# Kernel tuning notes

Hardware: AMD Instinct MI355X
Metric: run time of the kernel (lower is better)

The kernel has to match this reference:

```python
import jax, jax.numpy as jnp
import numpy as np

N = 100000   # nodes
E = 1600000  # edges
F_IN = 256   # input features
H = 128      # hidden
C = 40       # classes


def setup_inputs() -> dict:
    key = jax.random.key(0)
    ks = jax.random.split(key, 6)
    x = jax.random.normal(ks[0], (N, F_IN), dtype=jnp.float32)
    edge_index = jax.random.randint(ks[1], (2, E), 0, N, dtype=jnp.int32)
    edge_attr = jax.random.uniform(ks[2], (E,), dtype=jnp.float32)
    # Glorot-style init like GCNConv
    W1 = jax.random.normal(ks[3], (F_IN, H), dtype=jnp.float32) * (1.0 / np.sqrt(F_IN))
    b1 = jnp.zeros((H,), dtype=jnp.float32)
    W2 = jax.random.normal(ks[4], (H, C), dtype=jnp.float32) * (1.0 / np.sqrt(H))
    b2 = jnp.zeros((C,), dtype=jnp.float32)
    return {"x": x, "edge_index": edge_index, "edge_attr": edge_attr,
            "W1": W1, "b1": b1, "W2": W2, "b2": b2}


def _gcn_norm(edge_index, edge_weight, num_nodes):
    # PyG gcn_norm: add self-loops (weight 1), symmetric D^{-1/2} A D^{-1/2}
    row, col = edge_index[0], edge_index[1]
    loop = jnp.arange(num_nodes, dtype=row.dtype)
    row = jnp.concatenate([row, loop])
    col = jnp.concatenate([col, loop])
    ew = jnp.concatenate([edge_weight, jnp.ones((num_nodes,), edge_weight.dtype)])
    deg = jax.ops.segment_sum(ew, col, num_segments=num_nodes)
    dinv = jnp.where(deg > 0, jax.lax.rsqrt(deg), 0.0)
    norm = dinv[row] * ew * dinv[col]
    return row, col, norm


def _gcn_conv(x, row, col, norm, W, b):
    h = x @ W                              # [N, out] dense transform first
    msg = h[row] * norm[:, None]           # gather source + edge scaling
    out = jax.ops.segment_sum(msg, col, num_segments=x.shape[0])  # scatter-add
    return out + b


def reference(x, edge_index, edge_attr, W1, b1, W2, b2):
    row, col, norm = _gcn_norm(edge_index, edge_attr, x.shape[0])
    h = _gcn_conv(x, row, col, norm, W1, b1)
    h = jax.nn.relu(h)
    # dropout is identity in eval mode
    h = _gcn_conv(h, row, col, norm, W2, b2)
    return jax.nn.log_softmax(h, axis=1)
```

## Files before the change

### kernel.cpp

```cpp
#include <hip/hip_runtime.h>

#define N_NODES 100000
#define N_EDGES 1600000
#define F_INPUT 256
#define H_DIM   128
#define C_DIM   40
#define NB1     ((N_NODES + 255) / 256)
#define NGEMM1  1563
#define NCOUNT  1563
#define NMEGA   (NGEMM1 + NCOUNT)
#define PSTR    32

typedef short  bf8   __attribute__((ext_vector_type(8)));
typedef float  f32x4 __attribute__((ext_vector_type(4)));
typedef float  f32x2 __attribute__((ext_vector_type(2)));
typedef unsigned short u16x8 __attribute__((ext_vector_type(8)));

static __device__ __forceinline__ unsigned short f2bf(float f) {
    union { float f; unsigned u; } v; v.f = f;
    unsigned r = v.u + 0x7FFFu + ((v.u >> 16) & 1u);
    return (unsigned short)(r >> 16);
}
static __device__ __forceinline__ float bf2f(unsigned short b) {
    union { unsigned u; float f; } v; v.u = ((unsigned)b) << 16;
    return v.f;
}
static __device__ __forceinline__ f32x2 bfpair(unsigned u) {
    union { unsigned u; float f; } lo, hi;
    lo.u = u << 16; hi.u = u & 0xFFFF0000u;
    return (f32x2){lo.f, hi.f};
}

__global__ void k_pre(unsigned* packed, const float* __restrict__ W1,
                      const float* __restrict__ W2,
                      unsigned short* Wp1, unsigned short* Wp2) {
    if (blockIdx.x < NB1) {
        int i = blockIdx.x * 256 + threadIdx.x;
        if (i < N_NODES) packed[(size_t)i * PSTR] = (1u << 16);
        return;
    }
    int idx = (blockIdx.x - NB1) * 256 + threadIdx.x;
    if (idx < 32768) {
        int j = idx & 7, lane = (idx >> 3) & 63, ks = (idx >> 9) & 7, nt = idx >> 12;
        int m = lane & 15, q = lane >> 4;
        Wp1[idx] = f2bf(W1[(ks * 32 + q * 8 + j) * H_DIM + nt * 16 + m]);
    }
    int idx2 = idx - 32768;
    if (idx2 >= 0 && idx2 < 6144) {
        int j = idx2 & 7, lane = (idx2 >> 3) & 63, ks = (idx2 >> 9) & 3, nt = idx2 >> 11;
        int m = lane & 15, q = lane >> 4;
        int n = nt * 16 + m;
        Wp2[idx2] = (n < C_DIM) ? f2bf(W2[(ks * 32 + q * 8 + j) * C_DIM + n]) : (unsigned short)0;
    }
}

__global__ __launch_bounds__(256, 4) void k_mega(
        const float* __restrict__ x, const unsigned short* __restrict__ Wp,
        unsigned short* __restrict__ h,
        const int* __restrict__ col, const float* __restrict__ ea,
        unsigned* packed, int* __restrict__ rank) {
    __shared__ unsigned short lds_out[64 * H_DIM];
    int b = blockIdx.x;
    bool is_gemm = ((b & 1) == 0);
    if (!is_gemm) {
        int cb = b >> 1;
        int e0 = cb * 1024 + threadIdx.x;
        int cs[4]; unsigned qs[4]; unsigned old[4];
#pragma unroll
        for (int k = 0; k < 4; k++) {
            int e = e0 + k * 256;
            if (e < N_EDGES) {
                cs[k] = col[e];
                qs[k] = __float2uint_rn(ea[e] * 65536.0f);
            } else cs[k] = -1;
        }
#pragma unroll
        for (int k = 0; k < 4; k++)
            if (cs[k] >= 0)
                old[k] = atomicAdd(packed + (size_t)cs[k] * PSTR, (1u << 24) | qs[k]);
#pragma unroll
        for (int k = 0; k < 4; k++) {
            int e = e0 + k * 256;
            if (e < N_EDGES) rank[e] = (int)(old[k] >> 24);
        }
        return;
    }
    int tile = b >> 1;
    int tid = threadIdx.x;
    int wave = tid >> 6, lane = tid & 63;
    int m = lane & 15, q = lane >> 4;
    int row0 = tile * 64 + wave * 16;
    int rowA = row0 + m; if (rowA >= N_NODES) rowA = N_NODES - 1;

    f32x4 acc[8];
#pragma unroll
    for (int i = 0; i < 8; i++) acc[i] = (f32x4){0.f, 0.f, 0.f, 0.f};
    const float* xr = x + (long)rowA * F_INPUT + q * 8;
#pragma unroll
    for (int ks = 0; ks < 8; ks++) {
        float4 a0 = *(const float4*)(xr + ks * 32);
        float4 a1 = *(const float4*)(xr + ks * 32 + 4);
        bf8 a;
        a[0] = (short)f2bf(a0.x); a[1] = (short)f2bf(a0.y);
        a[2] = (short)f2bf(a0.z); a[3] = (short)f2bf(a0.w);
        a[4] = (short)f2bf(a1.x); a[5] = (short)f2bf(a1.y);
        a[6] = (short)f2bf(a1.z); a[7] = (short)f2bf(a1.w);
#pragma unroll
        for (int nt = 0; nt < 8; nt++) {
            bf8 bb = *(const bf8*)(Wp + (((nt * 8 + ks) * 64 + lane) << 3));
            acc[nt] = __builtin_amdgcn_mfma_f32_16x16x32_bf16(a, bb, acc[nt], 0, 0, 0);
        }
    }
    int lrow = wave * 16 + q * 4;
#pragma unroll
    for (int nt = 0; nt < 8; nt++)
#pragma unroll
        for (int r = 0; r < 4; r++)
            lds_out[(lrow + r) * H_DIM + nt * 16 + m] = f2bf(acc[nt][r]);
    __syncthreads();
    int valid = N_NODES - tile * 64; if (valid > 64) valid = 64;
    unsigned short* gbase = h + (size_t)tile * 64 * H_DIM;
#pragma unroll
    for (int i = 0; i < 4; i++) {
        int idx = (i * 256 + tid) * 8;
        if (idx < valid * H_DIM)
            *(u16x8*)(gbase + idx) = *(const u16x8*)(lds_out + idx);
    }
}

__global__ void k_scan1(const unsigned* __restrict__ packed, int* start, int* bsum,
                        float* dinv, int* __restrict__ cnt) {
    __shared__ int s[256];
    int i = blockIdx.x * 256 + threadIdx.x;
    unsigned pk = (i < N_NODES) ? packed[(size_t)i * PSTR] : 0;
    if (i < N_NODES) {
        dinv[i] = rsqrtf((float)(pk & 0xFFFFFFu) * (1.0f / 65536.0f));
        cnt[i] = (int)(pk >> 24);
    }
    int v = (int)(pk >> 24);
    s[threadIdx.x] = v; __syncthreads();
    for (int off = 1; off < 256; off <<= 1) {
        int t = (threadIdx.x >= off) ? s[threadIdx.x - off] : 0;
        __syncthreads();
        s[threadIdx.x] += t;
        __syncthreads();
    }
    if (i < N_NODES) start[i] = s[threadIdx.x] - v;
    if (threadIdx.x == 255) bsum[blockIdx.x] = s[255];
}

__global__ void k_scan2(int* bsum) {
    __shared__ int s[512];
    int v = (threadIdx.x < NB1) ? bsum[threadIdx.x] : 0;
    s[threadIdx.x] = v; __syncthreads();
    for (int off = 1; off < 512; off <<= 1) {
        int t = (threadIdx.x >= off) ? s[threadIdx.x - off] : 0;
        __syncthreads();
        s[threadIdx.x] += t;
        __syncthreads();
    }
    if (threadIdx.x < NB1) bsum[threadIdx.x] = s[threadIdx.x] - v;
}

__global__ void k_scatter(const int* __restrict__ row, const int* __restrict__ col,
                          const float* __restrict__ ea, const float* __restrict__ dinv,
                          const int* __restrict__ start, const int* __restrict__ bsum,
                          const int* __restrict__ rank, int2* __restrict__ csr) {
    int e = blockIdx.x * 256 + threadIdx.x;
    if (e < N_EDGES) {
        int c = col[e];
        int r = row[e];
        int pos = start[c] + bsum[c >> 8] + rank[e];
        float w = ea[e] * dinv[r];
        csr[pos] = make_int2(r, __float_as_int(w));
    }
}

__global__ void k_agg1(const unsigned short* __restrict__ h, const int2* __restrict__ csr,
                       const int* __restrict__ start, const int* __restrict__ bsum,
                       const int* __restrict__ cnt,
                       const float* __restrict__ dinv, const float* __restrict__ b1,
                       unsigned short* __restrict__ h1) {
    int c = (blockIdx.x * blockDim.x + threadIdx.x) >> 6;
    int lane = threadIdx.x & 63;
    if (c >= N_NODES) return;
    int eg = lane >> 4, cl = lane & 15;
    float di = dinv[c];
    int s = start[c] + bsum[c >> 8];
    int n = cnt[c];

    float w[5]; int r[5];
#pragma unroll
    for (int t = 0; t < 5; t++) {
        int i = eg + 4 * t;
        int2 p = csr[s + ((i < n) ? i : 0)];
        bool val = (i < n);
        r[t] = val ? p.x : c;
        w[t] = val ? __int_as_float(p.y) : 0.f;
    }
    uint4 gv[5];
#pragma unroll
    for (int t = 0; t < 5; t++)
        gv[t] = *(const uint4*)(h + (long)r[t] * H_DIM + cl * 8);
    uint4 selfv = (eg == 0) ? *(const uint4*)(h + (long)c * H_DIM + cl * 8)
                            : (uint4){0, 0, 0, 0};

    f32x2 acc[4];
#pragma unroll
    for (int k = 0; k < 4; k++) acc[k] = (f32x2){0.f, 0.f};
    {
        unsigned sv[4] = {selfv.x, selfv.y, selfv.z, selfv.w};
        f32x2 dd = (f32x2){di, di};
        if (eg == 0)
#pragma unroll
            for (int k = 0; k < 4; k++) acc[k] += dd * bfpair(sv[k]);
    }
#pragma unroll
    for (int t = 0; t < 5; t++) {
        unsigned vv[4] = {gv[t].x, gv[t].y, gv[t].z, gv[t].w};
        f32x2 ww = (f32x2){w[t], w[t]};
#pragma unroll
        for (int k = 0; k < 4; k++) acc[k] += ww * bfpair(vv[k]);
    }
    for (int i = 20 + eg; i < n; i += 4) {
        int2 p = csr[s + i];
        uint4 v4 = *(const uint4*)(h + (long)p.x * H_DIM + cl * 8);
        unsigned vv[4] = {v4.x, v4.y, v4.z, v4.w};
        float wt = __int_as_float(p.y);
        f32x2 ww = (f32x2){wt, wt};
#pragma unroll
        for (int k = 0; k < 4; k++) acc[k] += ww * bfpair(vv[k]);
    }
#pragma unroll
    for (int k = 0; k < 4; k++) {
        acc[k].x += __shfl_xor(acc[k].x, 16); acc[k].y += __shfl_xor(acc[k].y, 16);
        acc[k].x += __shfl_xor(acc[k].x, 32); acc[k].y += __shfl_xor(acc[k].y, 32);
    }
    if (eg == 0) {
        u16x8 o;
#pragma unroll
        for (int k = 0; k < 4; k++) {
            o[2 * k]     = f2bf(fmaxf(di * acc[k].x + b1[cl * 8 + 2 * k], 0.f));
            o[2 * k + 1] = f2bf(fmaxf(di * acc[k].y + b1[cl * 8 + 2 * k + 1], 0.f));
        }
        *(u16x8*)(h1 + (long)c * H_DIM + cl * 8) = o;
    }
}

__global__ __launch_bounds__(256, 4) void k_gemm2(const unsigned short* __restrict__ h1,
                        const unsigned short* __restrict__ Wp,
                        unsigned short* __restrict__ h2) {
    __shared__ unsigned short lds_out[64 * C_DIM];
    int tid = threadIdx.x;
    int wave = tid >> 6, lane = tid & 63;
    int m = lane & 15, q = lane >> 4;
    int row0 = blockIdx.x * 64 + wave * 16;
    int rowA = row0 + m; if (rowA >= N_NODES) rowA = N_NODES - 1;

    f32x4 acc[3];
#pragma unroll
    for (int i = 0; i < 3; i++) acc[i] = (f32x4){0.f, 0.f, 0.f, 0.f};
    const unsigned short* hr = h1 + (long)rowA * H_DIM + q * 8;
#pragma unroll
    for (int ks = 0; ks < 4; ks++) {
        bf8 a = *(const bf8*)(hr + ks * 32);
#pragma unroll
        for (int nt = 0; nt < 3; nt++) {
            bf8 b = *(const bf8*)(Wp + (((nt * 4 + ks) * 64 + lane) << 3));
            acc[nt] = __builtin_amdgcn_mfma_f32_16x16x32_bf16(a, b, acc[nt], 0, 0, 0);
        }
    }
    int lrow = wave * 16 + q * 4;
#pragma unroll
    for (int nt = 0; nt < 3; nt++)
#pragma unroll
        for (int r = 0; r < 4; r++) {
            int colo = nt * 16 + m;
            if (colo < C_DIM)
                lds_out[(lrow + r) * C_DIM + colo] = f2bf(acc[nt][r]);
        }
    __syncthreads();
    int valid = N_NODES - blockIdx.x * 64; if (valid > 64) valid = 64;
    unsigned short* gbase = h2 + (size_t)blockIdx.x * 64 * C_DIM;
    int total = valid * C_DIM;
#pragma unroll
    for (int i = 0; i < 3; i++) {
        int idx = (i * 256 + tid) * 4;
        if (idx < total)
            *(uint2*)(gbase + idx) = *(const uint2*)(lds_out + idx);
    }
}

__global__ void k_agg2(const unsigned short* __restrict__ h2, const int2* __restrict__ csr,
                       const int* __restrict__ start, const int* __restrict__ bsum,
                       const int* __restrict__ cnt,
                       const float* __restrict__ dinv, const float* __restrict__ b2,
                       float* __restrict__ out) {
    int c = (blockIdx.x * blockDim.x + threadIdx.x) >> 6;
    int lane = threadIdx.x & 63;
    if (c >= N_NODES) return;
    int eg = lane >> 3, cl = lane & 7;
    float di = dinv[c];
    int s = start[c] + bsum[c >> 8];
    int n = cnt[c];

    float w[3]; int r[3];
#pragma unroll
    for (int t = 0; t < 3; t++) {
        int i = eg + 8 * t;
        int2 p = csr[s + ((i < n) ? i : 0)];
        bool val = (i < n);
        r[t] = val ? p.x : c;
        w[t] = val ? __int_as_float(p.y) : 0.f;
    }
    uint4 gv[3] = {{0,0,0,0},{0,0,0,0},{0,0,0,0}};
    uint4 selfv = {0, 0, 0, 0};
    if (cl < 5) {
#pragma unroll
        for (int t = 0; t < 3; t++)
            gv[t] = *(const uint4*)(h2 + (long)r[t] * C_DIM + cl * 8);
        if (eg == 0) selfv = *(const uint4*)(h2 + (long)c * C_DIM + cl * 8);
    }
    f32x2 acc[4];
#pragma unroll
    for (int k = 0; k < 4; k++) acc[k] = (f32x2){0.f, 0.f};
    {
        unsigned sv[4] = {selfv.x, selfv.y, selfv.z, selfv.w};
        f32x2 dd = (f32x2){di, di};
        if (eg == 0 && cl < 5)
#pragma unroll
            for (int k = 0; k < 4; k++) acc[k] += dd * bfpair(sv[k]);
    }
#pragma unroll
    for (int t = 0; t < 3; t++) {
        unsigned vv[4] = {gv[t].x, gv[t].y, gv[t].z, gv[t].w};
        f32x2 ww = (f32x2){w[t], w[t]};
#pragma unroll
        for (int k = 0; k < 4; k++) acc[k] += ww * bfpair(vv[k]);
    }
    for (int i = 24 + eg; i < n; i += 8) {
        int2 p = csr[s + i];
        if (cl < 5) {
            uint4 v4 = *(const uint4*)(h2 + (long)p.x * C_DIM + cl * 8);
            unsigned vv[4] = {v4.x, v4.y, v4.z, v4.w};
            float wt = __int_as_float(p.y);
            f32x2 ww = (f32x2){wt, wt};
#pragma unroll
            for (int k = 0; k < 4; k++) acc[k] += ww * bfpair(vv[k]);
        }
    }
#pragma unroll
    for (int k = 0; k < 4; k++) {
        acc[k].x += __shfl_xor(acc[k].x, 8);  acc[k].y += __shfl_xor(acc[k].y, 8);
        acc[k].x += __shfl_xor(acc[k].x, 16); acc[k].y += __shfl_xor(acc[k].y, 16);
        acc[k].x += __shfl_xor(acc[k].x, 32); acc[k].y += __shfl_xor(acc[k].y, 32);
    }
    float v[8];
    float lm = -INFINITY;
    if (cl < 5) {
#pragma unroll
        for (int k = 0; k < 4; k++) {
            v[2 * k]     = di * acc[k].x + b2[cl * 8 + 2 * k];
            v[2 * k + 1] = di * acc[k].y + b2[cl * 8 + 2 * k + 1];
            lm = fmaxf(lm, fmaxf(v[2 * k], v[2 * k + 1]));
        }
    }
    lm = fmaxf(lm, __shfl_xor(lm, 1));
    lm = fmaxf(lm, __shfl_xor(lm, 2));
    lm = fmaxf(lm, __shfl_xor(lm, 4));
    float ls = 0.f;
    if (cl < 5) {
#pragma unroll
        for (int j = 0; j < 8; j++) ls += __expf(v[j] - lm);
    }
    ls += __shfl_xor(ls, 1);
    ls += __shfl_xor(ls, 2);
    ls += __shfl_xor(ls, 4);
    if (eg == 0 && cl < 5) {
        float lsm = lm + logf(ls);
        f32x4 o0, o1;
#pragma unroll
        for (int j = 0; j < 4; j++) { o0[j] = v[j] - lsm; o1[j] = v[j + 4] - lsm; }
        *(f32x4*)(out + (long)c * C_DIM + cl * 8)     = o0;
        *(f32x4*)(out + (long)c * C_DIM + cl * 8 + 4) = o1;
    }
}

extern "C" void kernel_launch(void* const* d_in, const int* in_sizes, int n_in,
                              void* d_out, int out_size, void* d_ws, size_t ws_size,
                              hipStream_t stream) {
    const float* x  = (const float*)d_in[0];
    const int*   ei = (const int*)d_in[1];
    const float* ea = (const float*)d_in[2];
    const float* W1 = (const float*)d_in[3];
    const float* b1 = (const float*)d_in[4];
    const float* W2 = (const float*)d_in[5];
    const float* b2 = (const float*)d_in[6];
    const int* row = ei;
    const int* col = ei + N_EDGES;

    char* ws = (char*)d_ws;
    size_t off = 0;
    auto alloc = [&](size_t bytes) -> void* {
        void* p = ws + off;
        off = (off + bytes + 255) & ~(size_t)255;
        return p;
    };
    unsigned*       packed = (unsigned*)alloc((size_t)N_NODES * PSTR * 4);
    float*          dinv   = (float*)alloc((size_t)N_NODES * 4);
    int*            rank   = (int*)alloc((size_t)N_EDGES * 4);
    int*            start  = (int*)alloc((size_t)N_NODES * 4);
    int*            bsum   = (int*)alloc(512 * 4);
    int*            cnt    = (int*)alloc((size_t)N_NODES * 4);
    int2*           csr    = (int2*)alloc((size_t)N_EDGES * 8);
    unsigned short* Wp1    = (unsigned short*)alloc(32768 * 2);
    unsigned short* Wp2    = (unsigned short*)alloc(6144 * 2);
    unsigned short* h      = (unsigned short*)alloc((size_t)(N_NODES + 64) * H_DIM * 2);
    unsigned short* h1     = (unsigned short*)alloc((size_t)N_NODES * H_DIM * 2);
    unsigned short* h2     = (unsigned short*)alloc((size_t)(N_NODES + 64) * C_DIM * 2);

    k_pre<<<NB1 + 152, 256, 0, stream>>>(packed, W1, W2, Wp1, Wp2);
    k_mega<<<NMEGA, 256, 0, stream>>>(x, Wp1, h, col, ea, packed, rank);
    k_scan1<<<NB1, 256, 0, stream>>>(packed, start, bsum, dinv, cnt);
    k_scan2<<<1, 512, 0, stream>>>(bsum);
    k_scatter<<<N_EDGES / 256, 256, 0, stream>>>(row, col, ea, dinv, start, bsum, rank, csr);
    k_agg1<<<N_NODES / 4, 256, 0, stream>>>(h, csr, start, bsum, cnt, dinv, b1, h1);
    k_gemm2<<<(N_NODES + 63) / 64, 256, 0, stream>>>(h1, Wp2, h2);
    k_agg2<<<N_NODES / 4, 256, 0, stream>>>(h2, csr, start, bsum, cnt, dinv, b2, (float*)d_out);
}
```

Before: 430.8 us.

## Replace global-atomic CSR build with two-pass bucketed radix-style sort

Replaces per-node global atomics on a padded packed counter array (with per-edge rank) with a two-level bucket sort. Per-chunk histograms over 256-node buckets are built in LDS, scanned, scattered into bucket-ordered records, then each bucket computes degrees, dinv and starts and places edges into CSR with LDS atomics. This removes heavily contended global atomics and random global writes. The cost is extra kernels, an extra 12.8MB intermediate record pass and several scans.

```diff
diff --git a/kernel.cpp b/kernel.cpp
--- a/kernel.cpp
+++ b/kernel.cpp
@@ -5,11 +5,9 @@
 #define F_INPUT 256
 #define H_DIM   128
 #define C_DIM   40
-#define NB1     ((N_NODES + 255) / 256)
-#define NGEMM1  1563
-#define NCOUNT  1563
-#define NMEGA   (NGEMM1 + NCOUNT)
-#define PSTR    32
+#define NBKT    391
+#define NCHK    1563
+#define NMEGA   (2 * NCHK)
 
 typedef short  bf8   __attribute__((ext_vector_type(8)));
 typedef float  f32x4 __attribute__((ext_vector_type(4)));
@@ -21,25 +19,15 @@
     unsigned r = v.u + 0x7FFFu + ((v.u >> 16) & 1u);
     return (unsigned short)(r >> 16);
 }
-static __device__ __forceinline__ float bf2f(unsigned short b) {
-    union { unsigned u; float f; } v; v.u = ((unsigned)b) << 16;
-    return v.f;
-}
 static __device__ __forceinline__ f32x2 bfpair(unsigned u) {
     union { unsigned u; float f; } lo, hi;
     lo.u = u << 16; hi.u = u & 0xFFFF0000u;
     return (f32x2){lo.f, hi.f};
 }
 
-__global__ void k_pre(unsigned* packed, const float* __restrict__ W1,
-                      const float* __restrict__ W2,
+__global__ void k_pre(const float* __restrict__ W1, const float* __restrict__ W2,
                       unsigned short* Wp1, unsigned short* Wp2) {
-    if (blockIdx.x < NB1) {
-        int i = blockIdx.x * 256 + threadIdx.x;
-        if (i < N_NODES) packed[(size_t)i * PSTR] = (1u << 16);
-        return;
-    }
-    int idx = (blockIdx.x - NB1) * 256 + threadIdx.x;
+    int idx = blockIdx.x * 256 + threadIdx.x;
     if (idx < 32768) {
         int j = idx & 7, lane = (idx >> 3) & 63, ks = (idx >> 9) & 7, nt = idx >> 12;
         int m = lane & 15, q = lane >> 4;
@@ -54,39 +42,29 @@
     }
 }
 
-__global__ __launch_bounds__(256, 4) void k_mega(
+__global__ __launch_bounds__(256, 4) void k_mega2(
         const float* __restrict__ x, const unsigned short* __restrict__ Wp,
         unsigned short* __restrict__ h,
-        const int* __restrict__ col, const float* __restrict__ ea,
-        unsigned* packed, int* __restrict__ rank) {
+        const int* __restrict__ col, unsigned* __restrict__ histG) {
     __shared__ unsigned short lds_out[64 * H_DIM];
     int b = blockIdx.x;
-    bool is_gemm = ((b & 1) == 0);
-    if (!is_gemm) {
-        int cb = b >> 1;
-        int e0 = cb * 1024 + threadIdx.x;
-        int cs[4]; unsigned qs[4]; unsigned old[4];
+    int tid = threadIdx.x;
+    if (b & 1) {
+        unsigned* histL = (unsigned*)lds_out;
+        int chunk = b >> 1;
+        for (int i = tid; i < NBKT; i += 256) histL[i] = 0;
+        __syncthreads();
+        int e0 = chunk * 1024 + tid;
 #pragma unroll
         for (int k = 0; k < 4; k++) {
             int e = e0 + k * 256;
-            if (e < N_EDGES) {
-                cs[k] = col[e];
-                qs[k] = __float2uint_rn(ea[e] * 65536.0f);
-            } else cs[k] = -1;
-        }
-#pragma unroll
-        for (int k = 0; k < 4; k++)
-            if (cs[k] >= 0)
-                old[k] = atomicAdd(packed + (size_t)cs[k] * PSTR, (1u << 24) | qs[k]);
-#pragma unroll
-        for (int k = 0; k < 4; k++) {
-            int e = e0 + k * 256;
-            if (e < N_EDGES) rank[e] = (int)(old[k] >> 24);
-        }
+            if (e < N_EDGES) atomicAdd(&histL[col[e] >> 8], 1u);
+        }
+        __syncthreads();
+        for (int i = tid; i < NBKT; i += 256) histG[(size_t)i * NCHK + chunk] = histL[i];
         return;
     }
     int tile = b >> 1;
-    int tid = threadIdx.x;
     int wave = tid >> 6, lane = tid & 63;
     int m = lane & 15, q = lane >> 4;
     int row0 = tile * 64 + wave * 16;
@@ -128,57 +106,137 @@
     }
 }
 
-__global__ void k_scan1(const unsigned* __restrict__ packed, int* start, int* bsum,
-                        float* dinv, int* __restrict__ cnt) {
-    __shared__ int s[256];
-    int i = blockIdx.x * 256 + threadIdx.x;
-    unsigned pk = (i < N_NODES) ? packed[(size_t)i * PSTR] : 0;
-    if (i < N_NODES) {
-        dinv[i] = rsqrtf((float)(pk & 0xFFFFFFu) * (1.0f / 65536.0f));
-        cnt[i] = (int)(pk >> 24);
-    }
-    int v = (int)(pk >> 24);
-    s[threadIdx.x] = v; __syncthreads();
+__global__ void k_scanB(unsigned* histG, unsigned* bktTotal) {
+    __shared__ unsigned s[256];
+    int B = blockIdx.x, t = threadIdx.x;
+    unsigned carry = 0;
+    for (int c0 = 0; c0 < NCHK; c0 += 256) {
+        int idx = c0 + t;
+        unsigned v = (idx < NCHK) ? histG[(size_t)B * NCHK + idx] : 0;
+        s[t] = v; __syncthreads();
+        for (int off = 1; off < 256; off <<= 1) {
+            unsigned u = (t >= off) ? s[t - off] : 0;
+            __syncthreads();
+            s[t] += u;
+            __syncthreads();
+        }
+        if (idx < NCHK) histG[(size_t)B * NCHK + idx] = s[t] - v + carry;
+        unsigned tot = s[255];
+        __syncthreads();
+        carry += tot;
+    }
+    if (t == 0) bktTotal[B] = carry;
+}
+
+__global__ void k_scanC(const unsigned* __restrict__ bktTotal, unsigned* bucketBase) {
+    __shared__ unsigned s[256];
+    int t = threadIdx.x;
+    unsigned carry = 0;
+    for (int c0 = 0; c0 < NBKT; c0 += 256) {
+        int idx = c0 + t;
+        unsigned v = (idx < NBKT) ? bktTotal[idx] : 0;
+        s[t] = v; __syncthreads();
+        for (int off = 1; off < 256; off <<= 1) {
+            unsigned u = (t >= off) ? s[t - off] : 0;
+            __syncthreads();
+            s[t] += u;
+            __syncthreads();
+        }
+        if (idx < NBKT) bucketBase[idx] = s[t] - v + carry;
+        unsigned tot = s[255];
+        __syncthreads();
+        carry += tot;
+    }
+    if (t == 0) bucketBase[NBKT] = carry;
+}
+
+__global__ void k_scat1(const int* __restrict__ row, const int* __restrict__ col,
+                        const float* __restrict__ ea,
+                        const unsigned* __restrict__ histG,
+                        const unsigned* __restrict__ bucketBase,
+                        int2* __restrict__ recs) {
+    __shared__ unsigned base_l[NBKT];
+    __shared__ unsigned cursor[NBKT];
+    int blk = blockIdx.x, t = threadIdx.x;
+    for (int i = t; i < NBKT; i += 256) {
+        base_l[i] = bucketBase[i] + histG[(size_t)i * NCHK + blk];
+        cursor[i] = 0;
+    }
+    __syncthreads();
+    int e0 = blk * 1024 + t;
+#pragma unroll
+    for (int k = 0; k < 4; k++) {
+        int e = e0 + k * 256;
+        if (e < N_EDGES) {
+            int c = col[e];
+            int bkt = c >> 8;
+            unsigned r = atomicAdd(&cursor[bkt], 1u);
+            int pos = (int)(base_l[bkt] + r);
+            recs[pos] = make_int2((row[e] << 8) | (c & 255), __float_as_int(ea[e]));
+        }
+    }
+}
+
+__global__ void k_pass2a(const int2* __restrict__ recs,
+                         const unsigned* __restrict__ bucketBase,
+                         int* __restrict__ start, int* __restrict__ cnt,
+                         float* __restrict__ dinv) {
+    __shared__ unsigned cntL[256];
+    __shared__ unsigned wsL[256];
+    __shared__ unsigned s[256];
+    int B = blockIdx.x, t = threadIdx.x;
+    cntL[t] = 0; wsL[t] = 0;
+    __syncthreads();
+    int lo = (int)bucketBase[B], hi = (int)bucketBase[B + 1];
+    for (int i = lo + t; i < hi; i += 256) {
+        int2 rc = recs[i];
+        int cl = rc.x & 255;
+        atomicAdd(&cntL[cl], 1u);
+        unsigned q = __float2uint_rn(__int_as_float(rc.y) * 65536.0f);
+        atomicAdd(&wsL[cl], q);
+    }
+    __syncthreads();
+    unsigned v = cntL[t];
+    s[t] = v; __syncthreads();
     for (int off = 1; off < 256; off <<= 1) {
-        int t = (threadIdx.x >= off) ? s[threadIdx.x - off] : 0;
-        __syncthreads();
-        s[threadIdx.x] += t;
-        __syncthreads();
-    }
-    if (i < N_NODES) start[i] = s[threadIdx.x] - v;
-    if (threadIdx.x == 255) bsum[blockIdx.x] = s[255];
-}
-
-__global__ void k_scan2(int* bsum) {
-    __shared__ int s[512];
-    int v = (threadIdx.x < NB1) ? bsum[threadIdx.x] : 0;
-    s[threadIdx.x] = v; __syncthreads();
-    for (int off = 1; off < 512; off <<= 1) {
-        int t = (threadIdx.x >= off) ? s[threadIdx.x - off] : 0;
-        __syncthreads();
-        s[threadIdx.x] += t;
-        __syncthreads();
-    }
-    if (threadIdx.x < NB1) bsum[threadIdx.x] = s[threadIdx.x] - v;
-}
-
-__global__ void k_scatter(const int* __restrict__ row, const int* __restrict__ col,
-                          const float* __restrict__ ea, const float* __restrict__ dinv,
-                          const int* __restrict__ start, const int* __restrict__ bsum,
-                          const int* __restrict__ rank, int2* __restrict__ csr) {
-    int e = blockIdx.x * 256 + threadIdx.x;
-    if (e < N_EDGES) {
-        int c = col[e];
-        int r = row[e];
-        int pos = start[c] + bsum[c >> 8] + rank[e];
-        float w = ea[e] * dinv[r];
-        csr[pos] = make_int2(r, __float_as_int(w));
+        unsigned u = (t >= off) ? s[t - off] : 0;
+        __syncthreads();
+        s[t] += u;
+        __syncthreads();
+    }
+    int node = B * 256 + t;
+    if (node < N_NODES) {
+        start[node] = (int)(bucketBase[B] + s[t] - v);
+        cnt[node] = (int)v;
+        dinv[node] = rsqrtf((float)(65536u + wsL[t]) * (1.0f / 65536.0f));
+    }
+}
+
+__global__ void k_pass2b(const int2* __restrict__ recs,
+                         const unsigned* __restrict__ bucketBase,
+                         const int* __restrict__ start,
+                         const float* __restrict__ dinv,
+                         int2* __restrict__ csr) {
+    __shared__ int startL[256];
+    __shared__ unsigned cur[256];
+    int B = blockIdx.x, t = threadIdx.x;
+    int node = B * 256 + t;
+    startL[t] = (node < N_NODES) ? start[node] : 0;
+    cur[t] = 0;
+    __syncthreads();
+    int lo = (int)bucketBase[B], hi = (int)bucketBase[B + 1];
+    for (int i = lo + t; i < hi; i += 256) {
+        int2 rc = recs[i];
+        int cl = rc.x & 255;
+        int rw = rc.x >> 8;
+        float w = __int_as_float(rc.y) * dinv[rw];
+        unsigned r = atomicAdd(&cur[cl], 1u);
+        csr[startL[cl] + (int)r] = make_int2(rw, __float_as_int(w));
     }
 }
 
 __global__ void k_agg1(const unsigned short* __restrict__ h, const int2* __restrict__ csr,
-                       const int* __restrict__ start, const int* __restrict__ bsum,
-                       const int* __restrict__ cnt,
+                       const int* __restrict__ start, const int* __restrict__ cnt,
                        const float* __restrict__ dinv, const float* __restrict__ b1,
                        unsigned short* __restrict__ h1) {
     int c = (blockIdx.x * blockDim.x + threadIdx.x) >> 6;
@@ -186,7 +244,7 @@
     if (c >= N_NODES) return;
     int eg = lane >> 4, cl = lane & 15;
     float di = dinv[c];
-    int s = start[c] + bsum[c >> 8];
+    int s = start[c];
     int n = cnt[c];
 
     float w[5]; int r[5];
@@ -292,8 +350,7 @@
 }
 
 __global__ void k_agg2(const unsigned short* __restrict__ h2, const int2* __restrict__ csr,
-                       const int* __restrict__ start, const int* __restrict__ bsum,
-                       const int* __restrict__ cnt,
+                       const int* __restrict__ start, const int* __restrict__ cnt,
                        const float* __restrict__ dinv, const float* __restrict__ b2,
                        float* __restrict__ out) {
     int c = (blockIdx.x * blockDim.x + threadIdx.x) >> 6;
@@ -301,7 +358,7 @@
     if (c >= N_NODES) return;
     int eg = lane >> 3, cl = lane & 7;
     float di = dinv[c];
-    int s = start[c] + bsum[c >> 8];
+    int s = start[c];
     int n = cnt[c];
 
     float w[3]; int r[3];
@@ -406,25 +463,28 @@
         off = (off + bytes + 255) & ~(size_t)255;
         return p;
     };
-    unsigned*       packed = (unsigned*)alloc((size_t)N_NODES * PSTR * 4);
-    float*          dinv   = (float*)alloc((size_t)N_NODES * 4);
-    int*            rank   = (int*)alloc((size_t)N_EDGES * 4);
-    int*            start  = (int*)alloc((size_t)N_NODES * 4);
-    int*            bsum   = (int*)alloc(512 * 4);
-    int*            cnt    = (int*)alloc((size_t)N_NODES * 4);
-    int2*           csr    = (int2*)alloc((size_t)N_EDGES * 8);
-    unsigned short* Wp1    = (unsigned short*)alloc(32768 * 2);
-    unsigned short* Wp2    = (unsigned short*)alloc(6144 * 2);
-    unsigned short* h      = (unsigned short*)alloc((size_t)(N_NODES + 64) * H_DIM * 2);
-    unsigned short* h1     = (unsigned short*)alloc((size_t)N_NODES * H_DIM * 2);
-    unsigned short* h2     = (unsigned short*)alloc((size_t)(N_NODES + 64) * C_DIM * 2);
-
-    k_pre<<<NB1 + 152, 256, 0, stream>>>(packed, W1, W2, Wp1, Wp2);
-    k_mega<<<NMEGA, 256, 0, stream>>>(x, Wp1, h, col, ea, packed, rank);
-    k_scan1<<<NB1, 256, 0, stream>>>(packed, start, bsum, dinv, cnt);
-    k_scan2<<<1, 512, 0, stream>>>(bsum);
-    k_scatter<<<N_EDGES / 256, 256, 0, stream>>>(row, col, ea, dinv, start, bsum, rank, csr);
-    k_agg1<<<N_NODES / 4, 256, 0, stream>>>(h, csr, start, bsum, cnt, dinv, b1, h1);
+    unsigned*       histG   = (unsigned*)alloc((size_t)NBKT * NCHK * 4);
+    unsigned*       bktTot  = (unsigned*)alloc((size_t)NBKT * 4);
+    unsigned*       bktBase = (unsigned*)alloc((size_t)(NBKT + 1) * 4);
+    int*            start   = (int*)alloc((size_t)N_NODES * 4);
+    int*            cnt     = (int*)alloc((size_t)N_NODES * 4);
+    float*          dinv    = (float*)alloc((size_t)N_NODES * 4);
+    int2*           recs    = (int2*)alloc((size_t)N_EDGES * 8);
+    int2*           csr     = (int2*)alloc((size_t)N_EDGES * 8);
+    unsigned short* Wp1     = (unsigned short*)alloc(32768 * 2);
+    unsigned short* Wp2     = (unsigned short*)alloc(6144 * 2);
+    unsigned short* h       = (unsigned short*)alloc((size_t)(N_NODES + 64) * H_DIM * 2);
+    unsigned short* h1      = (unsigned short*)alloc((size_t)N_NODES * H_DIM * 2);
+    unsigned short* h2      = (unsigned short*)alloc((size_t)(N_NODES + 64) * C_DIM * 2);
+
+    k_pre<<<152, 256, 0, stream>>>(W1, W2, Wp1, Wp2);
+    k_mega2<<<NMEGA, 256, 0, stream>>>(x, Wp1, h, col, histG);
+    k_scanB<<<NBKT, 256, 0, stream>>>(histG, bktTot);
+    k_scanC<<<1, 256, 0, stream>>>(bktTot, bktBase);
+    k_scat1<<<NCHK, 256, 0, stream>>>(row, col, ea, histG, bktBase, recs);
+    k_pass2a<<<NBKT, 256, 0, stream>>>(recs, bktBase, start, cnt, dinv);
+    k_pass2b<<<NBKT, 256, 0, stream>>>(recs, bktBase, start, dinv, csr);
+    k_agg1<<<N_NODES / 4, 256, 0, stream>>>(h, csr, start, cnt, dinv, b1, h1);
     k_gemm2<<<(N_NODES + 63) / 64, 256, 0, stream>>>(h1, Wp2, h2);
-    k_agg2<<<N_NODES / 4, 256, 0, stream>>>(h2, csr, start, bsum, cnt, dinv, b2, (float*)d_out);
-}
+    k_agg2<<<N_NODES / 4, 256, 0, stream>>>(h2, csr, start, cnt, dinv, b2, (float*)d_out);
+}
```

New measurement: 408.3 us. 1.06x faster.
